# Kernel optimization log

Measured on AMD Instinct MI355X. Metric: run time of the kernel, lower is better.

## Reference

```python
import jax, jax.numpy as jnp
import numpy as np

DEGREE = 12      # number of interior basis control dims
ORDER = 3        # cubic B-spline
V = 10           # number_variables
N = 65536        # batch
L = V * (V - 1) // 2          # 45 lambdas (strict lower triangle)
NCOEF = DEGREE + ORDER - 1    # 14 coefficients per lambda
LO, HI = -5.0, 5.0            # spline_range[:,0]


def make_knots():
    d = (HI - LO) / (DEGREE - 1)
    return jnp.linspace(LO - ORDER * d, HI + ORDER * d, DEGREE + 2 * ORDER, dtype=jnp.float32)


def bspline_basis(x, knots):
    # Cox-de Boor recursion, vectorized over all leading dims of x.
    # returns [..., NCOEF] basis values (len(knots) - ORDER - 1 functions).
    t = knots
    xe = x[..., None]
    B = ((xe >= t[:-1]) & (xe < t[1:])).astype(x.dtype)  # order-0 indicators
    for p in range(1, ORDER + 1):
        d1 = t[p:-1] - t[:-p - 1]
        d2 = t[p + 1:] - t[1:-p]
        a = jnp.where(d1 > 0, (xe - t[:-p - 1]) / jnp.where(d1 > 0, d1, 1.0), 0.0)
        b = jnp.where(d2 > 0, (t[p + 1:] - xe) / jnp.where(d2 > 0, d2, 1.0), 0.0)
        B = a * B[..., :-1] + b * B[..., 1:]
    return B


def setup_inputs() -> dict:
    key = jax.random.key(0)
    k1, k2 = jax.random.split(key)
    x = jax.random.normal(k1, (N, V), dtype=jnp.float32) * 2.0
    log_d = jnp.zeros((N, V), dtype=jnp.float32)
    params = 0.001 + 0.01 * jax.random.normal(k2, (NCOEF, L), dtype=jnp.float32)
    return {"x": x, "log_d": log_d, "params": params}


def reference(x, log_d, params):
    knots = make_knots()
    rows, cols = np.tril_indices(V, k=-1)  # var_num_list, covar_num_list
    # ReLULeR span restriction: clamp inputs into the spline range
    xc = jnp.clip(x[:, cols], LO, HI)              # [N, L]
    B = bspline_basis(xc, knots)                    # [N, L, NCOEF]
    lam = jnp.einsum('nlk,kl->nl', B, params)       # de Boor evaluation per pair
    # triangular lambda matrix: identity + scattered strict-lower entries
    eye = jnp.eye(V, dtype=x.dtype)
    M = jnp.broadcast_to(eye, (x.shape[0], V, V)).at[:, rows, cols].set(lam)
    out = jnp.einsum('nij,nj->ni', M, x)            # bmm(lambda_matrix, input)
    # ridge penalties on spline coefficients (penalize_towards=0)
    sec = jnp.sum(jnp.diff(params, n=2, axis=0) ** 2)
    fir = jnp.sum(jnp.diff(params, n=1, axis=0) ** 2)
    par = jnp.sum(params ** 2)
    return out, M, log_d, sec, fir, par
```

## Files before the change

### kernel.cpp

```cpp
#include <hip/hip_runtime.h>

#define V 10
#define L 45
#define NCOEF 14
#define NSAMP 65536
#define BS 16
#define NTHR 128
#define LAMP 46

typedef float v4f __attribute__((ext_vector_type(4)));

__global__ __launch_bounds__(NTHR, 8) void decor_fused(
    const float* __restrict__ x, const float* __restrict__ log_d,
    const float* __restrict__ params,
    float* __restrict__ out, float* __restrict__ Mout, float* __restrict__ logd_out,
    float* __restrict__ scal)
{
    __shared__ float ps[NCOEF * L];
    __shared__ float xs[BS * V];
    __shared__ float lam[BS * LAMP];

    const int tid = threadIdx.x;
    const int n0  = blockIdx.x * BS;

    for (int idx = tid; idx < NCOEF * L; idx += NTHR)
        ps[idx] = params[idx];
    const v4f* x4 = (const v4f*)(x + (size_t)n0 * V);
    for (int idx = tid; idx < BS * V / 4; idx += NTHR)
        ((v4f*)xs)[idx] = __builtin_nontemporal_load(&x4[idx]);
    const v4f* ld4  = (const v4f*)(log_d + (size_t)n0 * V);
    v4f*       ldo4 = (v4f*)(logd_out + (size_t)n0 * V);
    for (int idx = tid; idx < BS * V / 4; idx += NTHR)
        __builtin_nontemporal_store(__builtin_nontemporal_load(&ld4[idx]), &ldo4[idx]);

    __syncthreads();

    const float inv_d = 1.1f;
    const float c16   = 1.0f / 6.0f;
    v4f* M4 = (v4f*)(Mout + (size_t)n0 * V * V);
    for (int idx = tid; idx < BS * 25; idx += NTHR) {
        int nl = idx / 25;
        int q  = idx - nl * 25;
        int e  = q * 4;
        v4f v;
        #pragma unroll
        for (int t = 0; t < 4; ++t) {
            int ee = e + t;
            int i  = (ee * 205) >> 11;
            int j  = ee - 10 * i;
            float val;
            if (j > i)       val = 0.0f;
            else if (j == i) val = 1.0f;
            else {
                float xv = xs[nl * V + j];
                xv = fminf(fmaxf(xv, -5.0f), 5.0f);
                float u  = (xv + 5.0f) * inv_d + 3.0f;
                int   ii = (int)floorf(u);
                ii = max(3, min(ii, 14));
                float f  = u - (float)ii;
                float omf = 1.0f - f;
                float f2 = f * f, f3 = f2 * f;
                float N0 = omf * omf * omf * c16;
                float N1 = (3.0f * f3 - 6.0f * f2 + 4.0f) * c16;
                float N2 = (-3.0f * f3 + 3.0f * f2 + 3.0f * f + 1.0f) * c16;
                float N3 = f3 * c16;
                int l  = (i * (i - 1)) / 2 + j;
                int k0 = ii - 3;
                int k3 = min(k0 + 3, NCOEF - 1);
                val = N0 * ps[(k0    ) * L + l]
                    + N1 * ps[(k0 + 1) * L + l]
                    + N2 * ps[(k0 + 2) * L + l]
                    + N3 * ps[(k3    ) * L + l];
                lam[nl * LAMP + l] = val;
            }
            v[t] = val;
        }
        __builtin_nontemporal_store(v, &M4[idx]);
    }
    __syncthreads();

    for (int idx = tid; idx < BS * V; idx += NTHR) {
        int nl = idx / V;
        int i  = idx - nl * V;
        float acc = xs[idx];
        const float* lr = &lam[nl * LAMP + (i * (i - 1)) / 2];
        for (int j = 0; j < i; ++j)
            acc += lr[j] * xs[nl * V + j];
        __builtin_nontemporal_store(acc, &out[(size_t)n0 * V + idx]);
    }

    if (blockIdx.x == 0 && tid < 64) {
        float s_par = 0.f, s_fir = 0.f, s_sec = 0.f;
        for (int idx = tid; idx < NCOEF * L; idx += 64) {
            int k = idx / L;
            float p0 = ps[idx];
            s_par += p0 * p0;
            if (k + 1 < NCOEF) {
                float p1 = ps[idx + L];
                float d1 = p1 - p0;
                s_fir += d1 * d1;
                if (k + 2 < NCOEF) {
                    float p2 = ps[idx + 2 * L];
                    float d2 = p2 - 2.f * p1 + p0;
                    s_sec += d2 * d2;
                }
            }
        }
        for (int off = 32; off; off >>= 1) {
            s_sec += __shfl_down(s_sec, off);
            s_fir += __shfl_down(s_fir, off);
            s_par += __shfl_down(s_par, off);
        }
        if (tid == 0) { scal[0] = s_sec; scal[1] = s_fir; scal[2] = s_par; }
    }
}

extern "C" void kernel_launch(void* const* d_in, const int* in_sizes, int n_in,
                              void* d_out, int out_size, void* d_ws, size_t ws_size,
                              hipStream_t stream) {
    const float* x      = (const float*)d_in[0];
    const float* log_d  = (const float*)d_in[1];
    const float* params = (const float*)d_in[2];

    float* out      = (float*)d_out;
    float* M        = out + (size_t)NSAMP * V;
    float* logd_out = M + (size_t)NSAMP * V * V;
    float* scal     = logd_out + (size_t)NSAMP * V;

    decor_fused<<<NSAMP / BS, NTHR, 0, stream>>>(x, log_d, params, out, M, logd_out, scal);
}
```

Measured before the change: 21.26 us.

## Replace per-tile shared staging with a grid-stride flat work stream

The tiled kernel staged x and the lambdas in shared memory behind two barriers. It becomes a persistent grid-stride kernel over one flat index space covering the M float4 chunks, the log_d copy chunks and the per-sample output rows. Each output-row thread recomputes its sample's 45 lambdas in registers instead of reusing them from the M pass, which removes the barriers and shared staging at the cost of duplicated spline work. x is now read directly from global memory, and the per-sample out stores are strided and uncoalesced. Each wave loads params into shared memory itself with no block barrier, relying on in-order LDS access within a wave.

```diff
diff --git a/kernel.cpp b/kernel.cpp
--- a/kernel.cpp
+++ b/kernel.cpp
@@ -4,94 +4,29 @@
 #define L 45
 #define NCOEF 14
 #define NSAMP 65536
-#define BS 16
-#define NTHR 128
-#define LAMP 46
+#define NTHR 256
+#define NBLK 2048
 
 typedef float v4f __attribute__((ext_vector_type(4)));
 
-__global__ __launch_bounds__(NTHR, 8) void decor_fused(
+__global__ __launch_bounds__(NTHR) void decor_stream(
     const float* __restrict__ x, const float* __restrict__ log_d,
     const float* __restrict__ params,
     float* __restrict__ out, float* __restrict__ Mout, float* __restrict__ logd_out,
     float* __restrict__ scal)
 {
     __shared__ float ps[NCOEF * L];
-    __shared__ float xs[BS * V];
-    __shared__ float lam[BS * LAMP];
+    const int tid  = threadIdx.x;
+    const int lane = tid & 63;
 
-    const int tid = threadIdx.x;
-    const int n0  = blockIdx.x * BS;
+    for (int idx = lane; idx < NCOEF * L; idx += 64)
+        ps[idx] = params[idx];
 
-    for (int idx = tid; idx < NCOEF * L; idx += NTHR)
-        ps[idx] = params[idx];
-    const v4f* x4 = (const v4f*)(x + (size_t)n0 * V);
-    for (int idx = tid; idx < BS * V / 4; idx += NTHR)
-        ((v4f*)xs)[idx] = __builtin_nontemporal_load(&x4[idx]);
-    const v4f* ld4  = (const v4f*)(log_d + (size_t)n0 * V);
-    v4f*       ldo4 = (v4f*)(logd_out + (size_t)n0 * V);
-    for (int idx = tid; idx < BS * V / 4; idx += NTHR)
-        __builtin_nontemporal_store(__builtin_nontemporal_load(&ld4[idx]), &ldo4[idx]);
-
-    __syncthreads();
-
-    const float inv_d = 1.1f;
-    const float c16   = 1.0f / 6.0f;
-    v4f* M4 = (v4f*)(Mout + (size_t)n0 * V * V);
-    for (int idx = tid; idx < BS * 25; idx += NTHR) {
-        int nl = idx / 25;
-        int q  = idx - nl * 25;
-        int e  = q * 4;
-        v4f v;
-        #pragma unroll
-        for (int t = 0; t < 4; ++t) {
-            int ee = e + t;
-            int i  = (ee * 205) >> 11;
-            int j  = ee - 10 * i;
-            float val;
-            if (j > i)       val = 0.0f;
-            else if (j == i) val = 1.0f;
-            else {
-                float xv = xs[nl * V + j];
-                xv = fminf(fmaxf(xv, -5.0f), 5.0f);
-                float u  = (xv + 5.0f) * inv_d + 3.0f;
-                int   ii = (int)floorf(u);
-                ii = max(3, min(ii, 14));
-                float f  = u - (float)ii;
-                float omf = 1.0f - f;
-                float f2 = f * f, f3 = f2 * f;
-                float N0 = omf * omf * omf * c16;
-                float N1 = (3.0f * f3 - 6.0f * f2 + 4.0f) * c16;
-                float N2 = (-3.0f * f3 + 3.0f * f2 + 3.0f * f + 1.0f) * c16;
-                float N3 = f3 * c16;
-                int l  = (i * (i - 1)) / 2 + j;
-                int k0 = ii - 3;
-                int k3 = min(k0 + 3, NCOEF - 1);
-                val = N0 * ps[(k0    ) * L + l]
-                    + N1 * ps[(k0 + 1) * L + l]
-                    + N2 * ps[(k0 + 2) * L + l]
-                    + N3 * ps[(k3    ) * L + l];
-                lam[nl * LAMP + l] = val;
-            }
-            v[t] = val;
-        }
-        __builtin_nontemporal_store(v, &M4[idx]);
-    }
-    __syncthreads();
-
-    for (int idx = tid; idx < BS * V; idx += NTHR) {
-        int nl = idx / V;
-        int i  = idx - nl * V;
-        float acc = xs[idx];
-        const float* lr = &lam[nl * LAMP + (i * (i - 1)) / 2];
-        for (int j = 0; j < i; ++j)
-            acc += lr[j] * xs[nl * V + j];
-        __builtin_nontemporal_store(acc, &out[(size_t)n0 * V + idx]);
-    }
+    const float c16 = 1.0f / 6.0f;
 
     if (blockIdx.x == 0 && tid < 64) {
         float s_par = 0.f, s_fir = 0.f, s_sec = 0.f;
-        for (int idx = tid; idx < NCOEF * L; idx += 64) {
+        for (int idx = lane; idx < NCOEF * L; idx += 64) {
             int k = idx / L;
             float p0 = ps[idx];
             s_par += p0 * p0;
@@ -111,7 +46,88 @@
             s_fir += __shfl_down(s_fir, off);
             s_par += __shfl_down(s_par, off);
         }
-        if (tid == 0) { scal[0] = s_sec; scal[1] = s_fir; scal[2] = s_par; }
+        if (lane == 0) { scal[0] = s_sec; scal[1] = s_fir; scal[2] = s_par; }
+    }
+
+    const size_t NM4  = (size_t)NSAMP * 25;
+    const size_t NLD4 = (size_t)NSAMP * V / 4;
+    const size_t NTOT = NM4 + NLD4 + NSAMP;
+
+    for (size_t u = (size_t)blockIdx.x * NTHR + tid; u < NTOT;
+         u += (size_t)NBLK * NTHR) {
+        if (u < NM4) {
+            size_t n = u / 25;
+            int q  = (int)(u - n * 25);
+            int e0 = q * 4;
+            const float* xr = x + n * V;
+            v4f v;
+            #pragma unroll
+            for (int t = 0; t < 4; ++t) {
+                int ee = e0 + t;
+                int i  = (ee * 205) >> 11;
+                int j  = ee - 10 * i;
+                float val;
+                if (j > i)       val = 0.0f;
+                else if (j == i) val = 1.0f;
+                else {
+                    float xv = fminf(fmaxf(xr[j], -5.0f), 5.0f);
+                    float uu = (xv + 5.0f) * 1.1f + 3.0f;
+                    int   ii = (int)floorf(uu);
+                    ii = max(3, min(ii, 14));
+                    float f  = uu - (float)ii;
+                    float omf = 1.0f - f;
+                    float f2 = f * f, f3 = f2 * f;
+                    float N0 = omf * omf * omf * c16;
+                    float N1 = (3.f * f3 - 6.f * f2 + 4.f) * c16;
+                    float N2 = (-3.f * f3 + 3.f * f2 + 3.f * f + 1.f) * c16;
+                    float N3 = f3 * c16;
+                    int b  = (ii - 3) * L;
+                    int b3 = min(b + 3 * L, 13 * L);
+                    int l  = (i * (i - 1)) / 2 + j;
+                    val = N0 * ps[b + l] + N1 * ps[b + L + l]
+                        + N2 * ps[b + 2 * L + l] + N3 * ps[b3 + l];
+                }
+                v[t] = val;
+            }
+            __builtin_nontemporal_store(v, (v4f*)Mout + u);
+        } else if (u < NM4 + NLD4) {
+            size_t w = u - NM4;
+            __builtin_nontemporal_store(
+                __builtin_nontemporal_load((const v4f*)log_d + w),
+                (v4f*)logd_out + w);
+        } else {
+            size_t n = u - NM4 - NLD4;
+            const float* xr = x + n * V;
+            float xv[V], acc[V];
+            #pragma unroll
+            for (int j = 0; j < V; ++j) { xv[j] = xr[j]; acc[j] = xv[j]; }
+            #pragma unroll
+            for (int j = 0; j < V - 1; ++j) {
+                float xc = fminf(fmaxf(xv[j], -5.0f), 5.0f);
+                float uu = (xc + 5.0f) * 1.1f + 3.0f;
+                int   ii = (int)floorf(uu);
+                ii = max(3, min(ii, 14));
+                float f  = uu - (float)ii;
+                float omf = 1.0f - f;
+                float f2 = f * f, f3 = f2 * f;
+                float N0 = omf * omf * omf * c16;
+                float N1 = (3.f * f3 - 6.f * f2 + 4.f) * c16;
+                float N2 = (-3.f * f3 + 3.f * f2 + 3.f * f + 1.f) * c16;
+                float N3 = f3 * c16;
+                int b  = (ii - 3) * L;
+                int b3 = min(b + 3 * L, 13 * L);
+                #pragma unroll
+                for (int i = j + 1; i < V; ++i) {
+                    int l = (i * (i - 1)) / 2 + j;
+                    float lam = N0 * ps[b + l] + N1 * ps[b + L + l]
+                              + N2 * ps[b + 2 * L + l] + N3 * ps[b3 + l];
+                    acc[i] += lam * xv[j];
+                }
+            }
+            float* orow = out + n * V;
+            #pragma unroll
+            for (int i = 0; i < V; ++i) orow[i] = acc[i];
+        }
     }
 }
 
@@ -127,5 +143,5 @@
     float* logd_out = M + (size_t)NSAMP * V * V;
     float* scal     = logd_out + (size_t)NSAMP * V;
 
-    decor_fused<<<NSAMP / BS, NTHR, 0, stream>>>(x, log_d, params, out, M, logd_out, scal);
+    decor_stream<<<NBLK, NTHR, 0, stream>>>(x, log_d, params, out, M, logd_out, scal);
 }
```

After: 22.70 us. +6.8%, slower.
